# Kernel optimization log

Hardware: AMD Instinct MI355X
Metric: run time of the kernel (lower is better)

Reference implementation:

```python
import jax, jax.numpy as jnp
import numpy as np

N = 50000      # num nodes
E = 1_600_000  # num edges
D = 64         # in_dim == hidden_dim
H = 4          # heads
C = 16         # head_dim = hidden_dim // heads
NEG = 0.2      # leaky_relu negative slope (PyG GATConv default)


def setup_inputs() -> dict:
    key = jax.random.key(0)
    ks = jax.random.split(key, 20)
    f = lambda k, s: (jax.random.normal(k, s, jnp.float32) * 0.1)
    return dict(
        node_features=jax.random.normal(ks[0], (N, D), jnp.float32),
        edge_index=jax.random.randint(ks[1], (2, E), 0, N, dtype=jnp.int32),
        edge_type=jax.random.randint(ks[2], (E,), 0, 5, dtype=jnp.int32),
        edge_attr=jax.random.normal(ks[3], (E, 1), jnp.float32),
        # GAT layer 1 (PyG GATConv: lin has no bias, att_* are [H,C], final bias [H*C])
        W1=f(ks[4], (D, H * C)), att_src1=f(ks[5], (H, C)), att_dst1=f(ks[6], (H, C)),
        We1=f(ks[7], (1, H * C)), att_e1=f(ks[8], (H, C)), b1=jnp.zeros((H * C,), jnp.float32),
        # GAT layer 2
        W2=f(ks[9], (D, H * C)), att_src2=f(ks[10], (H, C)), att_dst2=f(ks[11], (H, C)),
        We2=f(ks[12], (1, H * C)), att_e2=f(ks[13], (H, C)), b2=jnp.zeros((H * C,), jnp.float32),
        # LayerNorms
        g1=jnp.ones((D,), jnp.float32), beta1=jnp.zeros((D,), jnp.float32),
        g2=jnp.ones((D,), jnp.float32), beta2=jnp.zeros((D,), jnp.float32),
        # output head
        Wout=f(ks[14], (D, 1)), bout=jnp.zeros((1,), jnp.float32),
    )


def _layernorm(x, g, b, eps=1e-5):
    mu = x.mean(-1, keepdims=True)
    v = ((x - mu) ** 2).mean(-1, keepdims=True)
    return (x - mu) * jax.lax.rsqrt(v + eps) * g + b


def _seg_softmax(alpha, dst, n):
    # numerically stable segment softmax over incoming edges of each dst node
    m = jax.ops.segment_max(alpha, dst, num_segments=n)
    m = jnp.where(jnp.isfinite(m), m, 0.0)
    ex = jnp.exp(alpha - m[dst])
    den = jax.ops.segment_sum(ex, dst, num_segments=n)
    return ex / (den[dst] + 1e-16)


def _gatconv(x, src, dst, eattr, W, a_s, a_d, We, a_e, b, n):
    xs = (x @ W).reshape(n, H, C)                       # [N,H,C]
    a_src = jnp.einsum('nhc,hc->nh', xs, a_s)           # [N,H]
    a_dst = jnp.einsum('nhc,hc->nh', xs, a_d)           # [N,H]
    ee = (eattr @ We).reshape(-1, H, C)                 # [E',H,C]
    a_edge = jnp.einsum('ehc,hc->eh', ee, a_e)          # [E',H]
    alpha = a_src[src] + a_dst[dst] + a_edge            # [E',H]
    alpha = jax.nn.leaky_relu(alpha, NEG)
    alpha = _seg_softmax(alpha, dst, n)                 # [E',H]
    msg = xs[src] * alpha[..., None]                    # [E',H,C] gather-weighted messages
    out = jax.ops.segment_sum(msg, dst, num_segments=n) # scatter-aggregate
    return out.reshape(n, H * C) + b


def reference(node_features, edge_index, edge_type, edge_attr,
              W1, att_src1, att_dst1, We1, att_e1, b1,
              W2, att_src2, att_dst2, We2, att_e2, b2,
              g1, beta1, g2, beta2, Wout, bout):
    src, dst = edge_index[0], edge_index[1]
    # PyG add_self_loops(fill_value='mean'): self-loop edge_attr = mean of edge_attr over incoming edges
    cnt = jax.ops.segment_sum(jnp.ones((E,), jnp.float32), dst, num_segments=N)
    loop_attr = jax.ops.segment_sum(edge_attr, dst, num_segments=N) / jnp.maximum(cnt, 1.0)[:, None]
    loops = jnp.arange(N, dtype=src.dtype)
    src2 = jnp.concatenate([src, loops])
    dst2 = jnp.concatenate([dst, loops])
    ea = jnp.concatenate([edge_attr, loop_attr], axis=0)

    residual = node_features  # in_dim == hidden_dim -> no res_proj
    h = _gatconv(node_features, src2, dst2, ea, W1, att_src1, att_dst1, We1, att_e1, b1, N)
    h = jax.nn.elu(_layernorm(h + residual, g1, beta1))
    residual = h
    h = _gatconv(h, src2, dst2, ea, W2, att_src2, att_dst2, We2, att_e2, b2, N)
    h = jax.nn.elu(_layernorm(h + residual, g2, beta2))
    return h @ Wout + bout
```

## Files before the change

### kernel.cpp

```cpp
#include <hip/hip_runtime.h>
#include <hip/hip_bf16.h>
#include <cfloat>

#define NN 50000
#define NE 1600000
#define NEG 0.2f
#define NBKT 392
#define BNODE 128
#define P1_TILE 2048
#define P1_BLOCKS 782
#define CAP 16
#define BCAP 4608
#define SLOTS 96
#define HSLOT 66
#define L2E 1.4426950408889634f

typedef __attribute__((ext_vector_type(8))) short bf8_t;
typedef __attribute__((ext_vector_type(4))) float f4_t;

__device__ __forceinline__ float bf16bits_to_f(unsigned v) {
  return __uint_as_float(v << 16);
}
__device__ __forceinline__ unsigned f_to_bf16bits(float f) {
  unsigned u = __float_as_uint(f);
  return (u + 0x7fffu + ((u >> 16) & 1u)) >> 16;
}

__global__ __launch_bounds__(256) void bin_kernel(
    const int* __restrict__ src, const int* __restrict__ dst,
    const float* __restrict__ ea, int* __restrict__ gcnt,
    int2* __restrict__ gbuf) {
  __shared__ int lcnt[NBKT];
  __shared__ int lbase[NBKT];
  __shared__ int2 lbuf[NBKT][CAP];
  int t = threadIdx.x;
  for (int i = t; i < NBKT; i += 256) lcnt[i] = 0;
  __syncthreads();
  int e0 = blockIdx.x * P1_TILE;
#pragma unroll
  for (int k = 0; k < P1_TILE / 256; ++k) {
    int e = e0 + k * 256 + t;
    if (e < NE) {
      int d = dst[e];
      int b = d >> 7;
      int2 v = make_int2(((d & 127) << 16) | src[e], __float_as_int(ea[e]));
      int pos = atomicAdd(&lcnt[b], 1);
      if (pos < CAP) {
        lbuf[b][pos] = v;
      } else {
        int gp = atomicAdd(&gcnt[b], 1);
        if (gp < BCAP) gbuf[(size_t)b * BCAP + gp] = v;
      }
    }
  }
  __syncthreads();
  for (int i = t; i < NBKT; i += 256) {
    int len = lcnt[i]; if (len > CAP) len = CAP;
    lbase[i] = atomicAdd(&gcnt[i], len);
  }
  __syncthreads();
  for (int sid = t; sid < NBKT * CAP; sid += 256) {
    int b = sid >> 4;
    int k = sid & (CAP - 1);
    int len = lcnt[b]; if (len > CAP) len = CAP;
    if (k < len) {
      int base = lbase[b];
      if (base + k < BCAP) gbuf[(size_t)b * BCAP + base + k] = lbuf[b][k];
    }
  }
}

__global__ __launch_bounds__(256) void build_kernel(
    const int* __restrict__ gcnt, const int2* __restrict__ gbuf,
    int* __restrict__ cnt, unsigned* __restrict__ csr) {
  __shared__ int lc[BNODE];
  int t = threadIdx.x;
  int b = blockIdx.x;
  if (t < BNODE) lc[t] = 0;
  __syncthreads();
  int len = gcnt[b]; if (len > BCAP) len = BCAP;
  const int2* buf = gbuf + (size_t)b * BCAP;
  for (int i = t; i < len; i += 256) {
    int2 v = buf[i];
    int dl = (v.x >> 16) & 127;
    int s = v.x & 0xffff;
    int pos = atomicAdd(&lc[dl], 1);
    if (pos < SLOTS) {
      unsigned eb = ((unsigned)v.y) & 0xffff0000u;
      csr[(size_t)(b * BNODE + dl) * SLOTS + pos] = eb | (unsigned)s;
    }
  }
  __syncthreads();
  if (t < BNODE) {
    int n = b * BNODE + t;
    if (n < NN) cnt[n] = min(lc[t], SLOTS);
  }
}

__global__ __launch_bounds__(256) void cvt_kernel(
    const float* __restrict__ x, unsigned short* __restrict__ xb) {
  size_t base = ((size_t)blockIdx.x * 256 + threadIdx.x) * 8;
  if (base >= (size_t)NN * 64) return;
  const float4* p = (const float4*)(x + base);
  float4 a = p[0], b = p[1];
  uint4 o;
  o.x = f_to_bf16bits(a.x) | (f_to_bf16bits(a.y) << 16);
  o.y = f_to_bf16bits(a.z) | (f_to_bf16bits(a.w) << 16);
  o.z = f_to_bf16bits(b.x) | (f_to_bf16bits(b.y) << 16);
  o.w = f_to_bf16bits(b.z) | (f_to_bf16bits(b.w) << 16);
  *(uint4*)(xb + base) = o;
}

__global__ __launch_bounds__(256) void gemm_mfma_kernel(
    const unsigned short* __restrict__ xb, const float* __restrict__ W,
    const float* __restrict__ att_s, const float* __restrict__ att_d,
    unsigned short* __restrict__ xsb, float* __restrict__ a_src,
    float* __restrict__ a_dst) {
  __shared__ unsigned short Wt[64][68];
  int t = threadIdx.x;
  for (int i = t; i < 4096; i += 256) {
    int k = i >> 6, n = i & 63;
    Wt[n][k] = (unsigned short)f_to_bf16bits(W[i]);
  }
  __syncthreads();
  int lane = t & 63, wave = t >> 6;
  int quad = lane >> 4, n16 = lane & 15;

  bf8_t bfrag[4][2];
#pragma unroll
  for (int nt = 0; nt < 4; ++nt)
#pragma unroll
    for (int kk = 0; kk < 2; ++kk)
      bfrag[nt][kk] = *(const bf8_t*)&Wt[nt * 16 + n16][kk * 32 + quad * 8];

  float as4[4], ad4[4];
#pragma unroll
  for (int nt = 0; nt < 4; ++nt) {
    as4[nt] = att_s[nt * 16 + n16];
    ad4[nt] = att_d[nt * 16 + n16];
  }

  int r0w = blockIdx.x * 128 + wave * 32;
#pragma unroll
  for (int tile = 0; tile < 2; ++tile) {
    int r0 = r0w + tile * 16;
    int rowA = r0 + n16; if (rowA > NN - 1) rowA = NN - 1;
    const bf8_t* xrow = (const bf8_t*)(xb + (size_t)rowA * 64);
    bf8_t af0 = xrow[quad];
    bf8_t af1 = xrow[4 + quad];
#pragma unroll
    for (int nt = 0; nt < 4; ++nt) {
      f4_t acc = {0.f, 0.f, 0.f, 0.f};
      acc = __builtin_amdgcn_mfma_f32_16x16x32_bf16(af0, bfrag[nt][0], acc, 0, 0, 0);
      acc = __builtin_amdgcn_mfma_f32_16x16x32_bf16(af1, bfrag[nt][1], acc, 0, 0, 0);
#pragma unroll
      for (int reg = 0; reg < 4; ++reg) {
        int row = r0 + quad * 4 + reg;
        float v = acc[reg];
        if (row < NN)
          xsb[(size_t)row * 64 + nt * 16 + n16] = (unsigned short)f_to_bf16bits(v);
        float p = v * as4[nt];
        float q = v * ad4[nt];
#pragma unroll
        for (int off = 8; off; off >>= 1) {
          p += __shfl_xor(p, off, 16);
          q += __shfl_xor(q, off, 16);
        }
        if (n16 == 0 && row < NN) {
          a_src[row * 4 + nt] = p * L2E;
          a_dst[row * 4 + nt] = q * L2E;
        }
      }
    }
  }
}

template <bool HEAD>
__global__ __launch_bounds__(256) void aggregate_kernel(
    const int* __restrict__ cnt, const unsigned* __restrict__ csr,
    const unsigned short* __restrict__ xsb, const float* __restrict__ a_src,
    const float* __restrict__ a_dst, const float* __restrict__ We,
    const float* __restrict__ att_e, const float* __restrict__ bias,
    const float* __restrict__ res, const float* __restrict__ g,
    const float* __restrict__ beta, const float* __restrict__ Wout,
    const float* __restrict__ bout, float* __restrict__ out,
    unsigned short* __restrict__ out_b) {
  __shared__ __align__(16) uint2 rec[4][4][HSLOT];
  int t = threadIdx.x;
  int lane = t & 63, wave = t >> 6;
  int n = blockIdx.x * 4 + wave;
  int h = lane >> 4;

  float sp = We[lane] * att_e[lane];
#pragma unroll
  for (int off = 8; off; off >>= 1) sp += __shfl_xor(sp, off, 16);
  sp *= L2E;
  float s0 = __shfl(sp, 0, 64), s1 = __shfl(sp, 16, 64);
  float s2 = __shfl(sp, 32, 64), s3 = __shfl(sp, 48, 64);

  const float4 adv = *(const float4*)(a_dst + (size_t)n * 4);

  int dn = cnt[n];
  int r0 = n * SLOTS, r1 = r0 + dn;
  float acc = 0.f, easum = 0.f, den = 0.f;
  const uint2* rp = &rec[wave][h][0];
  const unsigned short* xlane = xsb + lane;

  for (int base = r0; base < r1; base += 64) {
    int c = r1 - base; if (c > 64) c = 64;
    int e = base + lane;
    unsigned ce = (e < r1) ? csr[e] : 0u;
    float ea = __uint_as_float(ce & 0xffff0000u);
    easum += ea;
    unsigned soff = (ce & 0xffffu) * 128u;
    float ex0 = 0.f, ex1 = 0.f, ex2 = 0.f, ex3 = 0.f;
    if (e < r1) {
      const float4 av = *(const float4*)(a_src + (size_t)(ce & 0xffffu) * 4);
      float a0 = av.x + fmaf(ea, s0, adv.x); a0 = fmaxf(a0, NEG * a0);
      float a1 = av.y + fmaf(ea, s1, adv.y); a1 = fmaxf(a1, NEG * a1);
      float a2 = av.z + fmaf(ea, s2, adv.z); a2 = fmaxf(a2, NEG * a2);
      float a3 = av.w + fmaf(ea, s3, adv.w); a3 = fmaxf(a3, NEG * a3);
      ex0 = exp2f(a0); ex1 = exp2f(a1); ex2 = exp2f(a2); ex3 = exp2f(a3);
    }
    rec[wave][0][lane] = make_uint2(soff, __float_as_uint(ex0));
    rec[wave][1][lane] = make_uint2(soff, __float_as_uint(ex1));
    rec[wave][2][lane] = make_uint2(soff, __float_as_uint(ex2));
    rec[wave][3][lane] = make_uint2(soff, __float_as_uint(ex3));
    int c4 = (c + 3) & ~3;
    for (int j = 0; j < c4; j += 4) {
      uint2 v0 = rp[j], v1 = rp[j + 1], v2 = rp[j + 2], v3 = rp[j + 3];
      float xv0 = bf16bits_to_f(*(const unsigned short*)((const char*)xlane + v0.x));
      float xv1 = bf16bits_to_f(*(const unsigned short*)((const char*)xlane + v1.x));
      float xv2 = bf16bits_to_f(*(const unsigned short*)((const char*)xlane + v2.x));
      float xv3 = bf16bits_to_f(*(const unsigned short*)((const char*)xlane + v3.x));
      float e0f = __uint_as_float(v0.y), e1f = __uint_as_float(v1.y);
      float e2f = __uint_as_float(v2.y), e3f = __uint_as_float(v3.y);
      den += e0f + e1f + e2f + e3f;
      acc = fmaf(e0f, xv0, acc);
      acc = fmaf(e1f, xv1, acc);
      acc = fmaf(e2f, xv2, acc);
      acc = fmaf(e3f, xv3, acc);
    }
  }

#pragma unroll
  for (int off = 32; off; off >>= 1) easum += __shfl_xor(easum, off, 64);
  float adn = (h == 0) ? adv.x : (h == 1) ? adv.y : (h == 2) ? adv.z : adv.w;

  float loop_ea = easum / fmaxf((float)dn, 1.0f);
  float as_h = a_src[(size_t)n * 4 + h];
  float a_self = as_h + fmaf(loop_ea, sp, adn);
  a_self = fmaxf(a_self, NEG * a_self);
  float ex_self = exp2f(a_self);
  den += ex_self;
  acc = fmaf(ex_self, bf16bits_to_f(xsb[(size_t)n * 64 + lane]), acc);

  float v = acc / (den + 1e-16f) + bias[lane] + res[(size_t)n * 64 + lane];
  float mu = v;
#pragma unroll
  for (int off = 32; off; off >>= 1) mu += __shfl_xor(mu, off, 64);
  mu *= (1.0f / 64.0f);
  float d = v - mu;
  float var = d * d;
#pragma unroll
  for (int off = 32; off; off >>= 1) var += __shfl_xor(var, off, 64);
  var *= (1.0f / 64.0f);
  float y = d * rsqrtf(var + 1e-5f) * g[lane] + beta[lane];
  y = y > 0.f ? y : expm1f(y);
  if (HEAD) {
    float p = y * Wout[lane];
#pragma unroll
    for (int off = 32; off; off >>= 1) p += __shfl_xor(p, off, 64);
    if (lane == 0) out[n] = p + bout[0];
  } else {
    out[(size_t)n * 64 + lane] = y;
    out_b[(size_t)n * 64 + lane] = (unsigned short)f_to_bf16bits(y);
  }
}

extern "C" void kernel_launch(void* const* d_in, const int* in_sizes, int n_in,
                              void* d_out, int out_size, void* d_ws,
                              size_t ws_size, hipStream_t stream) {
  const float* node_features = (const float*)d_in[0];
  const int* edge_index = (const int*)d_in[1];
  const int* src = edge_index;
  const int* dst = edge_index + NE;
  const float* edge_attr = (const float*)d_in[3];
  const float* W1 = (const float*)d_in[4];
  const float* att_src1 = (const float*)d_in[5];
  const float* att_dst1 = (const float*)d_in[6];
  const float* We1 = (const float*)d_in[7];
  const float* att_e1 = (const float*)d_in[8];
  const float* b1 = (const float*)d_in[9];
  const float* W2 = (const float*)d_in[10];
  const float* att_src2 = (const float*)d_in[11];
  const float* att_dst2 = (const float*)d_in[12];
  const float* We2 = (const float*)d_in[13];
  const float* att_e2 = (const float*)d_in[14];
  const float* b2 = (const float*)d_in[15];
  const float* g1 = (const float*)d_in[16];
  const float* beta1 = (const float*)d_in[17];
  const float* g2 = (const float*)d_in[18];
  const float* beta2 = (const float*)d_in[19];
  const float* Wout = (const float*)d_in[20];
  const float* bout = (const float*)d_in[21];
  float* out = (float*)d_out;

  char* ws = (char*)d_ws;
  size_t o = 0;
  auto alloc = [&](size_t bytes) {
    void* p = ws + o;
    o += (bytes + 255) & ~(size_t)255;
    return p;
  };
  int* gcnt = (int*)alloc((size_t)NBKT * 4);
  int2* gbuf = (int2*)alloc((size_t)NBKT * BCAP * 8);
  int* cnt = (int*)alloc((size_t)NN * 4);
  unsigned* csr = (unsigned*)alloc((size_t)NN * SLOTS * 4);
  unsigned short* xb = (unsigned short*)alloc((size_t)NN * 64 * 2);
  unsigned short* xsb = (unsigned short*)alloc((size_t)NN * 64 * 2);
  unsigned short* h1b = (unsigned short*)alloc((size_t)NN * 64 * 2);
  float* a_srcb = (float*)alloc((size_t)NN * 4 * 4);
  float* a_dstb = (float*)alloc((size_t)NN * 4 * 4);
  float* h1 = (float*)alloc((size_t)NN * 64 * 4);

  hipMemsetAsync(gcnt, 0, (size_t)NBKT * 4, stream);

  bin_kernel<<<P1_BLOCKS, 256, 0, stream>>>(src, dst, edge_attr, gcnt, gbuf);
  build_kernel<<<NBKT, 256, 0, stream>>>(gcnt, gbuf, cnt, csr);

  cvt_kernel<<<1563, 256, 0, stream>>>(node_features, xb);
  gemm_mfma_kernel<<<391, 256, 0, stream>>>(xb, W1, att_src1, att_dst1, xsb,
                                            a_srcb, a_dstb);
  aggregate_kernel<false><<<NN / 4, 256, 0, stream>>>(
      cnt, csr, xsb, a_srcb, a_dstb, We1, att_e1, b1, node_features, g1, beta1,
      nullptr, nullptr, h1, h1b);

  gemm_mfma_kernel<<<391, 256, 0, stream>>>(h1b, W2, att_src2, att_dst2, xsb,
                                            a_srcb, a_dstb);
  aggregate_kernel<true><<<NN / 4, 256, 0, stream>>>(
      cnt, csr, xsb, a_srcb, a_dstb, We2, att_e2, b2, h1, g2, beta2, Wout, bout,
      out, nullptr);
}
```

Baseline: 280.4 us.

## Fuse fp32-to-bf16 conversion into GEMM and split edges across half-waves in aggregation

The separate cvt kernel and its bf16 scratch buffer are removed. The first GEMM now reads fp32 node features and packs them to bf16 in registers. The aggregation kernel is reorganized so each lane gathers two bf16 features as one 32-bit load, and the two half-waves process alternating edges, with partial sums combined by a cross-half shuffle. This halves the per-wave gather iterations and drops one launch plus a round trip through memory, at the cost of extra shuffles and the duplicated sums in the LayerNorm and head reductions being rescaled.

```diff
diff --git a/kernel.cpp b/kernel.cpp
--- a/kernel.cpp
+++ b/kernel.cpp
@@ -12,7 +12,6 @@
 #define CAP 16
 #define BCAP 4608
 #define SLOTS 96
-#define HSLOT 66
 #define L2E 1.4426950408889634f
 
 typedef __attribute__((ext_vector_type(8))) short bf8_t;
@@ -97,22 +96,16 @@
   }
 }
 
-__global__ __launch_bounds__(256) void cvt_kernel(
-    const float* __restrict__ x, unsigned short* __restrict__ xb) {
-  size_t base = ((size_t)blockIdx.x * 256 + threadIdx.x) * 8;
-  if (base >= (size_t)NN * 64) return;
-  const float4* p = (const float4*)(x + base);
-  float4 a = p[0], b = p[1];
-  uint4 o;
-  o.x = f_to_bf16bits(a.x) | (f_to_bf16bits(a.y) << 16);
-  o.y = f_to_bf16bits(a.z) | (f_to_bf16bits(a.w) << 16);
-  o.z = f_to_bf16bits(b.x) | (f_to_bf16bits(b.y) << 16);
-  o.w = f_to_bf16bits(b.z) | (f_to_bf16bits(b.w) << 16);
-  *(uint4*)(xb + base) = o;
-}
-
+__device__ __forceinline__ bf8_t pack8(const float* p) {
+  bf8_t r;
+#pragma unroll
+  for (int i = 0; i < 8; ++i) r[i] = (short)f_to_bf16bits(p[i]);
+  return r;
+}
+
+template <bool FP32IN>
 __global__ __launch_bounds__(256) void gemm_mfma_kernel(
-    const unsigned short* __restrict__ xb, const float* __restrict__ W,
+    const void* __restrict__ xin, const float* __restrict__ W,
     const float* __restrict__ att_s, const float* __restrict__ att_d,
     unsigned short* __restrict__ xsb, float* __restrict__ a_src,
     float* __restrict__ a_dst) {
@@ -145,9 +138,17 @@
   for (int tile = 0; tile < 2; ++tile) {
     int r0 = r0w + tile * 16;
     int rowA = r0 + n16; if (rowA > NN - 1) rowA = NN - 1;
-    const bf8_t* xrow = (const bf8_t*)(xb + (size_t)rowA * 64);
-    bf8_t af0 = xrow[quad];
-    bf8_t af1 = xrow[4 + quad];
+    bf8_t af0, af1;
+    if (FP32IN) {
+      const float* xr = (const float*)xin + (size_t)rowA * 64 + quad * 8;
+      af0 = pack8(xr);
+      af1 = pack8(xr + 32);
+    } else {
+      const bf8_t* xrow =
+          (const bf8_t*)((const unsigned short*)xin + (size_t)rowA * 64);
+      af0 = xrow[quad];
+      af1 = xrow[4 + quad];
+    }
 #pragma unroll
     for (int nt = 0; nt < 4; ++nt) {
       f4_t acc = {0.f, 0.f, 0.f, 0.f};
@@ -185,11 +186,13 @@
     const float* __restrict__ beta, const float* __restrict__ Wout,
     const float* __restrict__ bout, float* __restrict__ out,
     unsigned short* __restrict__ out_b) {
-  __shared__ __align__(16) uint2 rec[4][4][HSLOT];
+  __shared__ __align__(16) uint2 rec[4][64][4];
   int t = threadIdx.x;
   int lane = t & 63, wave = t >> 6;
   int n = blockIdx.x * 4 + wave;
-  int h = lane >> 4;
+  int d2 = lane & 31;
+  int hb = d2 >> 3;
+  int half = lane >> 5;
 
   float sp = We[lane] * att_e[lane];
 #pragma unroll
@@ -202,9 +205,9 @@
 
   int dn = cnt[n];
   int r0 = n * SLOTS, r1 = r0 + dn;
-  float acc = 0.f, easum = 0.f, den = 0.f;
-  const uint2* rp = &rec[wave][h][0];
-  const unsigned short* xlane = xsb + lane;
+  float accx = 0.f, accy = 0.f, den = 0.f, easum = 0.f;
+  const uint2* rpb = &rec[wave][half][hb];
+  const char* xd = (const char*)xsb + d2 * 4;
 
   for (int base = r0; base < r1; base += 64) {
     int c = r1 - base; if (c > 64) c = 64;
@@ -222,59 +225,73 @@
       float a3 = av.w + fmaf(ea, s3, adv.w); a3 = fmaxf(a3, NEG * a3);
       ex0 = exp2f(a0); ex1 = exp2f(a1); ex2 = exp2f(a2); ex3 = exp2f(a3);
     }
-    rec[wave][0][lane] = make_uint2(soff, __float_as_uint(ex0));
-    rec[wave][1][lane] = make_uint2(soff, __float_as_uint(ex1));
-    rec[wave][2][lane] = make_uint2(soff, __float_as_uint(ex2));
-    rec[wave][3][lane] = make_uint2(soff, __float_as_uint(ex3));
+    uint4* wp = (uint4*)&rec[wave][lane][0];
+    wp[0] = make_uint4(soff, __float_as_uint(ex0), soff, __float_as_uint(ex1));
+    wp[1] = make_uint4(soff, __float_as_uint(ex2), soff, __float_as_uint(ex3));
     int c4 = (c + 3) & ~3;
     for (int j = 0; j < c4; j += 4) {
-      uint2 v0 = rp[j], v1 = rp[j + 1], v2 = rp[j + 2], v3 = rp[j + 3];
-      float xv0 = bf16bits_to_f(*(const unsigned short*)((const char*)xlane + v0.x));
-      float xv1 = bf16bits_to_f(*(const unsigned short*)((const char*)xlane + v1.x));
-      float xv2 = bf16bits_to_f(*(const unsigned short*)((const char*)xlane + v2.x));
-      float xv3 = bf16bits_to_f(*(const unsigned short*)((const char*)xlane + v3.x));
-      float e0f = __uint_as_float(v0.y), e1f = __uint_as_float(v1.y);
-      float e2f = __uint_as_float(v2.y), e3f = __uint_as_float(v3.y);
-      den += e0f + e1f + e2f + e3f;
-      acc = fmaf(e0f, xv0, acc);
-      acc = fmaf(e1f, xv1, acc);
-      acc = fmaf(e2f, xv2, acc);
-      acc = fmaf(e3f, xv3, acc);
-    }
-  }
-
+      uint2 va = rpb[j * 4];
+      uint2 vb = rpb[j * 4 + 8];
+      unsigned ua = *(const unsigned*)(xd + va.x);
+      unsigned ub = *(const unsigned*)(xd + vb.x);
+      float efa = __uint_as_float(va.y), efb = __uint_as_float(vb.y);
+      den += efa + efb;
+      accx = fmaf(efa, __uint_as_float(ua << 16), accx);
+      accy = fmaf(efa, __uint_as_float(ua & 0xffff0000u), accy);
+      accx = fmaf(efb, __uint_as_float(ub << 16), accx);
+      accy = fmaf(efb, __uint_as_float(ub & 0xffff0000u), accy);
+    }
+  }
+
+  den += __shfl_xor(den, 32, 64);
+  accx += __shfl_xor(accx, 32, 64);
+  accy += __shfl_xor(accy, 32, 64);
 #pragma unroll
   for (int off = 32; off; off >>= 1) easum += __shfl_xor(easum, off, 64);
-  float adn = (h == 0) ? adv.x : (h == 1) ? adv.y : (h == 2) ? adv.z : adv.w;
 
   float loop_ea = easum / fmaxf((float)dn, 1.0f);
-  float as_h = a_src[(size_t)n * 4 + h];
-  float a_self = as_h + fmaf(loop_ea, sp, adn);
+  float as_h = a_src[(size_t)n * 4 + hb];
+  float adn = (hb == 0) ? adv.x : (hb == 1) ? adv.y : (hb == 2) ? adv.z : adv.w;
+  float sph = (hb == 0) ? s0 : (hb == 1) ? s1 : (hb == 2) ? s2 : s3;
+  float a_self = as_h + fmaf(loop_ea, sph, adn);
   a_self = fmaxf(a_self, NEG * a_self);
   float ex_self = exp2f(a_self);
   den += ex_self;
-  acc = fmaf(ex_self, bf16bits_to_f(xsb[(size_t)n * 64 + lane]), acc);
-
-  float v = acc / (den + 1e-16f) + bias[lane] + res[(size_t)n * 64 + lane];
-  float mu = v;
-#pragma unroll
-  for (int off = 32; off; off >>= 1) mu += __shfl_xor(mu, off, 64);
-  mu *= (1.0f / 64.0f);
-  float d = v - mu;
-  float var = d * d;
+  unsigned un = *(const unsigned*)((const char*)xsb + (size_t)n * 128 + d2 * 4);
+  accx = fmaf(ex_self, __uint_as_float(un << 16), accx);
+  accy = fmaf(ex_self, __uint_as_float(un & 0xffff0000u), accy);
+
+  float rden = 1.f / (den + 1e-16f);
+  const float2 bi = *(const float2*)(bias + d2 * 2);
+  const float2 rsd = *(const float2*)(res + (size_t)n * 64 + d2 * 2);
+  float vx = accx * rden + bi.x + rsd.x;
+  float vy = accy * rden + bi.y + rsd.y;
+  float s = vx + vy;
+#pragma unroll
+  for (int off = 32; off; off >>= 1) s += __shfl_xor(s, off, 64);
+  float mu = s * (1.0f / 128.0f);
+  float dx = vx - mu, dy = vy - mu;
+  float var = dx * dx + dy * dy;
 #pragma unroll
   for (int off = 32; off; off >>= 1) var += __shfl_xor(var, off, 64);
-  var *= (1.0f / 64.0f);
-  float y = d * rsqrtf(var + 1e-5f) * g[lane] + beta[lane];
-  y = y > 0.f ? y : expm1f(y);
+  var *= (1.0f / 128.0f);
+  float rstd = rsqrtf(var + 1e-5f);
+  const float2 gg = *(const float2*)(g + d2 * 2);
+  const float2 bb = *(const float2*)(beta + d2 * 2);
+  float yx = dx * rstd * gg.x + bb.x;
+  float yy = dy * rstd * gg.y + bb.y;
+  yx = yx > 0.f ? yx : expm1f(yx);
+  yy = yy > 0.f ? yy : expm1f(yy);
   if (HEAD) {
-    float p = y * Wout[lane];
+    const float2 wv = *(const float2*)(Wout + d2 * 2);
+    float p = yx * wv.x + yy * wv.y;
 #pragma unroll
     for (int off = 32; off; off >>= 1) p += __shfl_xor(p, off, 64);
-    if (lane == 0) out[n] = p + bout[0];
-  } else {
-    out[(size_t)n * 64 + lane] = y;
-    out_b[(size_t)n * 64 + lane] = (unsigned short)f_to_bf16bits(y);
+    if (lane == 0) out[n] = p * 0.5f + bout[0];
+  } else if (lane < 32) {
+    *(float2*)(out + (size_t)n * 64 + d2 * 2) = make_float2(yx, yy);
+    unsigned ob = f_to_bf16bits(yx) | (f_to_bf16bits(yy) << 16);
+    *(unsigned*)(out_b + (size_t)n * 64 + d2 * 2) = ob;
   }
 }
 
@@ -317,7 +334,6 @@
   int2* gbuf = (int2*)alloc((size_t)NBKT * BCAP * 8);
   int* cnt = (int*)alloc((size_t)NN * 4);
   unsigned* csr = (unsigned*)alloc((size_t)NN * SLOTS * 4);
-  unsigned short* xb = (unsigned short*)alloc((size_t)NN * 64 * 2);
   unsigned short* xsb = (unsigned short*)alloc((size_t)NN * 64 * 2);
   unsigned short* h1b = (unsigned short*)alloc((size_t)NN * 64 * 2);
   float* a_srcb = (float*)alloc((size_t)NN * 4 * 4);
@@ -329,15 +345,14 @@
   bin_kernel<<<P1_BLOCKS, 256, 0, stream>>>(src, dst, edge_attr, gcnt, gbuf);
   build_kernel<<<NBKT, 256, 0, stream>>>(gcnt, gbuf, cnt, csr);
 
-  cvt_kernel<<<1563, 256, 0, stream>>>(node_features, xb);
-  gemm_mfma_kernel<<<391, 256, 0, stream>>>(xb, W1, att_src1, att_dst1, xsb,
-                                            a_srcb, a_dstb);
+  gemm_mfma_kernel<true><<<391, 256, 0, stream>>>(
+      node_features, W1, att_src1, att_dst1, xsb, a_srcb, a_dstb);
   aggregate_kernel<false><<<NN / 4, 256, 0, stream>>>(
       cnt, csr, xsb, a_srcb, a_dstb, We1, att_e1, b1, node_features, g1, beta1,
       nullptr, nullptr, h1, h1b);
 
-  gemm_mfma_kernel<<<391, 256, 0, stream>>>(h1b, W2, att_src2, att_dst2, xsb,
-                                            a_srcb, a_dstb);
+  gemm_mfma_kernel<false><<<391, 256, 0, stream>>>(
+      h1b, W2, att_src2, att_dst2, xsb, a_srcb, a_dstb);
   aggregate_kernel<true><<<NN / 4, 256, 0, stream>>>(
       cnt, csr, xsb, a_srcb, a_dstb, We2, att_e2, b2, h1, g2, beta2, Wout, bout,
       out, nullptr);
```

New measurement: 277.3 us. About the same (-1.1%).
